# Optimization experiments

Hardware: AMD Instinct MI355X
Metric: run time of the kernel (lower is better)

Reference implementation:

```python
import jax, jax.numpy as jnp
import numpy as np

# Dims: N tokens, D input, H expert hidden, O output, E experts, G gate hidden, K top-k
N, D, H, O, E, G, K = 8192, 1024, 2048, 1024, 8, 256, 2
BALANCE_COEF = 0.01


def setup_inputs() -> dict:
    key = jax.random.key(0)
    ks = jax.random.split(key, 12)
    def lin(k, shape, fan_in):
        return jax.random.normal(k, shape, jnp.float32) * (1.0 / np.sqrt(fan_in))
    return {
        "x":   jax.random.normal(ks[0], (N, D), jnp.float32),
        # gating MLP: D -> G -> E
        "Wg1": lin(ks[1], (D, G), D), "bg1": jnp.zeros((G,), jnp.float32),
        "Wg2": lin(ks[2], (G, E), G), "bg2": jnp.zeros((E,), jnp.float32),
        # stacked expert MLPs: D -> H -> H -> O (ExpertNetwork, num_layers=2)
        "W1": lin(ks[3], (E, D, H), D), "b1": jnp.zeros((E, H), jnp.float32),
        "W2": lin(ks[4], (E, H, H), H), "b2": jnp.zeros((E, H), jnp.float32),
        "W3": lin(ks[5], (E, H, O), H), "b3": jnp.zeros((E, O), jnp.float32),
    }


def reference(x, Wg1, bg1, Wg2, bg2, W1, b1, W2, b2, W3, b3):
    # Gating: 2-layer MLP -> softmax -> top-k -> renormalize (eval: no noise/dropout)
    logits = jnp.maximum(x @ Wg1 + bg1, 0.0) @ Wg2 + bg2            # [N, E]
    probs = jax.nn.softmax(logits, axis=-1)
    w, idx = jax.lax.top_k(probs, K)                                # [N, K]
    w = w / jnp.sum(w, axis=-1, keepdims=True)
    onehot = jax.nn.one_hot(idx, E, dtype=x.dtype)                  # [N, K, E]
    comb = jnp.sum(onehot * w[..., None], axis=1)                   # [N, E] per-token expert weight

    # Dense-equivalent combine: unselected tokens get weight 0, identical math to
    # the masked dispatch + scatter-add in the torch code.
    def expert_step(acc, params):
        W1e, b1e, W2e, b2e, W3e, b3e, we = params                   # we: [N]
        h = jnp.maximum(x @ W1e + b1e, 0.0)                         # [N, H]
        h = jnp.maximum(h @ W2e + b2e, 0.0)                         # [N, H]
        o = h @ W3e + b3e                                           # [N, O]
        return acc + o * we[:, None], None

    out, _ = jax.lax.scan(expert_step, jnp.zeros((N, O), x.dtype),
                          (W1, b1, W2, b2, W3, b3, comb.T))

    # aux losses: expert_usage[e] = sum_i mean_b(indices[b,i]==e)
    expert_usage = jnp.sum(onehot, axis=(0, 1)) / N                 # [E]
    balance_loss = jnp.mean((expert_usage - 1.0 / E) ** 2) * BALANCE_COEF
    return out, balance_loss, expert_usage
```

## Files before the change

### kernel.cpp

```cpp
#include <hip/hip_runtime.h>
#include <hip/hip_bf16.h>
#include <cstdint>
#include <cstddef>

#define N_TOK 8192
#define D_IN  1024
#define H_DIM 2048
#define O_DIM 1024
#define E_NUM 8
#define G_DIM 256
#define MAXT256 72
#define MAXT128 144
#define MAXROWS (MAXT256*256)

typedef __attribute__((ext_vector_type(8))) __bf16 bf16x8;
typedef __attribute__((ext_vector_type(4))) float floatx4;

#define GCAST(p) ((__attribute__((address_space(1))) void*)(void*)(p))
#define LCAST(p) ((__attribute__((address_space(3))) void*)(p))

#define JOB_G1_END   512
#define JOB_CAST_END 4608
#define JOB_W1_END   8704

__device__ inline void transpose_body(const float* __restrict__ src,
                                      __bf16* __restrict__ dst,
                                      int K, int N, int e, int ktile, int ntile,
                                      float* smemf) {
  float (*tl)[64] = (float(*)[64])smemf;
  const float* s = src + (size_t)e * K * N;
  __bf16* d = dst + (size_t)e * K * N;
  int k0 = ktile * 64, n0 = ntile * 64;
  int t = threadIdx.x;
  int kr = t >> 4, nc = t & 15;
#pragma unroll
  for (int p = 0; p < 4; p++) {
    int r = kr + p * 16;
    float4 v = *reinterpret_cast<const float4*>(
        s + (size_t)(k0 + r) * N + n0 + nc * 4);
    *reinterpret_cast<float4*>(&tl[r][(nc * 4 + 8 * (r >> 3)) & 63]) = v;
  }
  __syncthreads();
  int n = t >> 3, kg = t & 7;
#pragma unroll
  for (int p = 0; p < 2; p++) {
    int c = n + p * 32;
    bf16x8 o;
#pragma unroll
    for (int j = 0; j < 8; j++)
      o[j] = (__bf16)tl[kg * 8 + j][(c + 8 * kg) & 63];
    *reinterpret_cast<bf16x8*>(d + (size_t)(n0 + c) * K + k0 + kg * 8) = o;
  }
}

__device__ inline void gate1_body(const float* __restrict__ x,
                                  const float* __restrict__ Wg1,
                                  const float* __restrict__ bg1,
                                  float* __restrict__ g,
                                  int bn, int bm, float* smemf) {
  float (*As)[68] = (float(*)[68])smemf;
  float (*Bs)[68] = (float(*)[68])(smemf + 32 * 68);
  int t = threadIdx.x;
  int tm = t >> 4, tn = t & 15;
  float acc[4][4] = {};
  for (int k0 = 0; k0 < D_IN; k0 += 32) {
#pragma unroll
    for (int i = 0; i < 2; i++) {
      int idx = t + 256 * i;
      int row = idx >> 3, c4 = idx & 7;
      float4 v = *reinterpret_cast<const float4*>(
          x + (size_t)(bm * 64 + row) * D_IN + k0 + c4 * 4);
      As[c4 * 4 + 0][row] = v.x;
      As[c4 * 4 + 1][row] = v.y;
      As[c4 * 4 + 2][row] = v.z;
      As[c4 * 4 + 3][row] = v.w;
      int brow = idx >> 4, bc4 = idx & 15;
      float4 wv = *reinterpret_cast<const float4*>(
          Wg1 + (size_t)(k0 + brow) * G_DIM + bn * 64 + bc4 * 4);
      *reinterpret_cast<float4*>(&Bs[brow][bc4 * 4]) = wv;
    }
    __syncthreads();
#pragma unroll
    for (int k = 0; k < 32; k++) {
      float4 av = *reinterpret_cast<const float4*>(&As[k][tm * 4]);
      float4 bv = *reinterpret_cast<const float4*>(&Bs[k][tn * 4]);
      float a4[4] = {av.x, av.y, av.z, av.w};
      float b4[4] = {bv.x, bv.y, bv.z, bv.w};
#pragma unroll
      for (int r = 0; r < 4; r++)
#pragma unroll
        for (int c = 0; c < 4; c++) acc[r][c] = fmaf(a4[r], b4[c], acc[r][c]);
    }
    __syncthreads();
  }
  int gr = bm * 64 + tm * 4, gc = bn * 64 + tn * 4;
#pragma unroll
  for (int r = 0; r < 4; r++) {
    float4 o;
    o.x = fmaxf(acc[r][0] + bg1[gc + 0], 0.f);
    o.y = fmaxf(acc[r][1] + bg1[gc + 1], 0.f);
    o.z = fmaxf(acc[r][2] + bg1[gc + 2], 0.f);
    o.w = fmaxf(acc[r][3] + bg1[gc + 3], 0.f);
    *reinterpret_cast<float4*>(g + (size_t)(gr + r) * G_DIM + gc) = o;
  }
}

__global__ __launch_bounds__(256) void prep_kernel(
    const float* __restrict__ x, __bf16* __restrict__ xb,
    const float* __restrict__ W1, __bf16* __restrict__ W1t,
    const float* __restrict__ Wg1, const float* __restrict__ bg1,
    float* __restrict__ g) {
  __shared__ float smemf[4352];
  int b = blockIdx.x;
  if (b < JOB_G1_END) {
    gate1_body(x, Wg1, bg1, g, b & 3, b >> 2, smemf);
  } else if (b < JOB_CAST_END) {
    int id = b - JOB_G1_END;
    int i = id * 2048 + threadIdx.x * 8;
    float4 v0 = *reinterpret_cast<const float4*>(x + i);
    float4 v1 = *reinterpret_cast<const float4*>(x + i + 4);
    bf16x8 o;
    o[0] = (__bf16)v0.x; o[1] = (__bf16)v0.y; o[2] = (__bf16)v0.z; o[3] = (__bf16)v0.w;
    o[4] = (__bf16)v1.x; o[5] = (__bf16)v1.y; o[6] = (__bf16)v1.z; o[7] = (__bf16)v1.w;
    *reinterpret_cast<bf16x8*>(xb + i) = o;
  } else {
    int id = b - JOB_CAST_END;
    transpose_body(W1, W1t, D_IN, H_DIM, id >> 9, (id >> 5) & 15, id & 31, smemf);
  }
}

__global__ __launch_bounds__(256) void gate2_kernel(const float* __restrict__ g,
                                                    const float* __restrict__ Wg2,
                                                    const float* __restrict__ bg2,
                                                    int* __restrict__ top_idx,
                                                    float* __restrict__ top_w,
                                                    int* __restrict__ counts) {
  __shared__ float lg[32][9];
  int t = threadIdx.x;
  int tl = t >> 3, e = t & 7;
  int n = blockIdx.x * 32 + tl;
  const float* gr = g + (size_t)n * G_DIM;
  float acc = bg2[e];
  for (int i = 0; i < G_DIM; i += 4) {
    float4 v = *reinterpret_cast<const float4*>(gr + i);
    acc += v.x * Wg2[(i + 0) * E_NUM + e];
    acc += v.y * Wg2[(i + 1) * E_NUM + e];
    acc += v.z * Wg2[(i + 2) * E_NUM + e];
    acc += v.w * Wg2[(i + 3) * E_NUM + e];
  }
  lg[tl][e] = acc;
  __syncthreads();
  if (e == 0) {
    float l[8];
#pragma unroll
    for (int i = 0; i < 8; i++) l[i] = lg[tl][i];
    int i0 = 0;
    for (int i = 1; i < 8; i++)
      if (l[i] > l[i0]) i0 = i;
    int i1 = (i0 == 0) ? 1 : 0;
    for (int i = 0; i < 8; i++)
      if (i != i0 && l[i] > l[i1]) i1 = i;
    float d = expf(l[i1] - l[i0]);
    float w0 = 1.f / (1.f + d);
    float w1 = d * w0;
    top_idx[n * 2 + 0] = i0;
    top_idx[n * 2 + 1] = i1;
    top_w[n * 2 + 0] = w0;
    top_w[n * 2 + 1] = w1;
    atomicAdd(&counts[i0], 1);
    atomicAdd(&counts[i1], 1);
  }
}

__global__ void g3_kernel(const int* __restrict__ counts, int* __restrict__ cursors,
                          int* __restrict__ off_pad, int* __restrict__ nt128,
                          int* __restrict__ nt256,
                          int* __restrict__ meta128, int* __restrict__ meta256,
                          float* __restrict__ out_tail,
                          int* __restrict__ slot_token) {
  if (threadIdx.x == 0) {
    int off = 0, n2 = 0, n1 = 0;
    float mse = 0.f;
    for (int e = 0; e < E_NUM; e++) {
      off_pad[e] = off;
      int c = counts[e];
      int tiles = (c + 255) >> 8;
      for (int i = 0; i < tiles; i++) {
        int s0 = off + i * 256;
        meta256[n2 * 2 + 0] = e; meta256[n2 * 2 + 1] = s0; n2++;
        meta128[n1 * 2 + 0] = e; meta128[n1 * 2 + 1] = s0; n1++;
        meta128[n1 * 2 + 0] = e; meta128[n1 * 2 + 1] = s0 + 128; n1++;
      }
      off += tiles << 8;
      cursors[e] = 0;
      float u = (float)c / (float)N_TOK;
      out_tail[1 + e] = u;
      float dd = u - 0.125f;
      mse += dd * dd;
    }
    *nt256 = n2;
    *nt128 = n1;
    out_tail[0] = (mse / 8.0f) * 0.01f;
  }
  for (int s = threadIdx.x; s < MAXROWS; s += 256) slot_token[s] = 0;
}

__global__ __launch_bounds__(256) void scatter_kernel(const int* __restrict__ top_idx,
                                                      const int* __restrict__ off_pad,
                                                      int* __restrict__ cursors,
                                                      int* __restrict__ slot_token,
                                                      int* __restrict__ token_slots) {
  int n = blockIdx.x * 256 + threadIdx.x;
#pragma unroll
  for (int k = 0; k < 2; k++) {
    int e = top_idx[n * 2 + k];
    int pos = atomicAdd(&cursors[e], 1);
    int s = off_pad[e] + pos;
    slot_token[s] = n;
    token_slots[n * 2 + k] = s;
  }
}

__global__ __launch_bounds__(256) void moe_gemm_kernel(
    const __bf16* __restrict__ A, int Astride,
    const __bf16* __restrict__ Wt, const float* __restrict__ bias,
    int Kdim, int Ndim,
    const int* __restrict__ tile_meta, const int* __restrict__ ntiles_p,
    const int* __restrict__ slot_token,
    __bf16* __restrict__ h_out,
    const float* __restrict__ W2src, __bf16* __restrict__ W2dst,
    const float* __restrict__ W3src, __bf16* __restrict__ W3dst) {
  __shared__ __align__(16) char smem[32768];
  int tile = blockIdx.y;
  if (tile >= MAXT128) {
    int id = (tile - MAXT128) * gridDim.x + blockIdx.x;
    if (id < 8192) {
      transpose_body(W2src, W2dst, H_DIM, H_DIM, id >> 10, (id >> 5) & 31,
                     id & 31, (float*)smem);
    } else {
      id -= 8192;
      transpose_body(W3src, W3dst, H_DIM, O_DIM, id >> 9, (id >> 4) & 31,
                     id & 15, (float*)smem);
    }
    return;
  }
  if (tile >= *ntiles_p) return;
  __bf16* As = (__bf16*)smem;
  __bf16* Bs = (__bf16*)(smem + 16384);
  int ex = tile_meta[tile * 2 + 0];
  int slot0 = tile_meta[tile * 2 + 1];
  int n0 = blockIdx.x * 128;
  int t = threadIdx.x, l = t & 63, w = t >> 6;

  size_t aoff[4], boff[4];
#pragma unroll
  for (int i = 0; i < 4; i++) {
    int gidx = (w * 4 + i) * 64 + l;
    int row = gidx >> 3;
    int kch = (gidx & 7) ^ (row & 7);
    int sl = slot0 + row;
    long long rb = (long long)slot_token[sl] * Astride;
    aoff[i] = (size_t)rb + kch * 8;
    boff[i] = ((size_t)ex * Ndim + n0 + row) * (size_t)Kdim + kch * 8;
  }

  int wm = (w >> 1) * 64, wn = (w & 1) * 64;
  int lm = l & 15, lq = l >> 4;
  floatx4 acc[4][4] = {};

  for (int k0 = 0; k0 < Kdim; k0 += 64) {
#pragma unroll
    for (int i = 0; i < 4; i++) {
      __builtin_amdgcn_global_load_lds(GCAST(A + aoff[i] + k0),
                                       LCAST((char*)As + w * 4096 + i * 1024),
                                       16, 0, 0);
      __builtin_amdgcn_global_load_lds(GCAST(Wt + boff[i] + k0),
                                       LCAST((char*)Bs + w * 4096 + i * 1024),
                                       16, 0, 0);
    }
    __syncthreads();
#pragma unroll
    for (int half = 0; half < 2; half++) {
      bf16x8 af[4], bfr[4];
#pragma unroll
      for (int i = 0; i < 4; i++) {
        int r = wm + i * 16 + lm;
        int s = (half * 4 + lq) ^ (r & 7);
        af[i] = *reinterpret_cast<const bf16x8*>(As + r * 64 + s * 8);
      }
#pragma unroll
      for (int j = 0; j < 4; j++) {
        int r = wn + j * 16 + lm;
        int s = (half * 4 + lq) ^ (r & 7);
        bfr[j] = *reinterpret_cast<const bf16x8*>(Bs + r * 64 + s * 8);
      }
#pragma unroll
      for (int i = 0; i < 4; i++)
#pragma unroll
        for (int j = 0; j < 4; j++)
          acc[i][j] = __builtin_amdgcn_mfma_f32_16x16x32_bf16(af[i], bfr[j],
                                                              acc[i][j], 0, 0, 0);
    }
    __syncthreads();
  }

  float bcol[4];
#pragma unroll
  for (int j = 0; j < 4; j++) bcol[j] = bias[(size_t)ex * Ndim + n0 + wn + j * 16 + lm];
#pragma unroll
  for (int i = 0; i < 4; i++) {
#pragma unroll
    for (int r = 0; r < 4; r++) {
      int sl = slot0 + wm + i * 16 + lq * 4 + r;
      __bf16* hrow = h_out + (size_t)sl * Ndim + n0 + wn + lm;
#pragma unroll
      for (int j = 0; j < 4; j++) {
        float v = fmaxf(acc[i][j][r] + bcol[j], 0.f);
        hrow[j * 16] = (__bf16)v;
      }
    }
  }
}

__global__ __launch_bounds__(512) void moe_gemm256_kernel(
    const __bf16* __restrict__ A,
    const __bf16* __restrict__ Wt, const float* __restrict__ bias,
    int Kdim, int Ndim,
    const int* __restrict__ tile_meta, const int* __restrict__ ntiles_p,
    __bf16* __restrict__ h_out, float* __restrict__ y_out, int finalMode) {
  __shared__ __align__(16) char smem[131072];
  int tile = blockIdx.y;
  if (tile >= *ntiles_p) return;
  int ex = tile_meta[tile * 2 + 0];
  int slot0 = tile_meta[tile * 2 + 1];
  int n0 = blockIdx.x * 256;
  int t = threadIdx.x, l = t & 63, w = t >> 6;
  int wm2 = w >> 2, wn4 = w & 3;
  int lm = l & 15, lq = l >> 4;

  size_t aoff[2][2], boff[2][2];
#pragma unroll
  for (int h = 0; h < 2; h++)
#pragma unroll
    for (int i = 0; i < 2; i++) {
      int gidx = i * 512 + t;
      int row = gidx >> 3;
      int kch = (gidx & 7) ^ (row & 7);
      aoff[h][i] = (size_t)(slot0 + h * 128 + row) * (size_t)Kdim + kch * 8;
      boff[h][i] = ((size_t)ex * Ndim + n0 + h * 128 + row) * (size_t)Kdim + kch * 8;
    }

  floatx4 acc[8][4] = {};

  auto SA = [&](int kt, int h, int d) {
    char* dst = smem + d * 65536 + h * 16384;
#pragma unroll
    for (int i = 0; i < 2; i++)
      __builtin_amdgcn_global_load_lds(GCAST(A + aoff[h][i] + (size_t)kt * 64),
                                       LCAST(dst + i * 8192 + w * 1024), 16, 0, 0);
  };
  auto SB = [&](int kt, int h, int d) {
    char* dst = smem + d * 65536 + 32768 + h * 16384;
#pragma unroll
    for (int i = 0; i < 2; i++)
      __builtin_amdgcn_global_load_lds(GCAST(Wt + boff[h][i] + (size_t)kt * 64),
                                       LCAST(dst + i * 8192 + w * 1024), 16, 0, 0);
  };

  int NKT = Kdim >> 6;
  int NIT = NKT >> 1;

  asm volatile("s_waitcnt vmcnt(0)" ::: "memory");
  SA(0, 0, 0); SA(0, 1, 0); SB(0, 0, 0); SB(0, 1, 0);
  SB(1, 0, 1); SB(1, 1, 1);
  asm volatile("s_waitcnt vmcnt(4)" ::: "memory");
  __builtin_amdgcn_s_barrier();
  __builtin_amdgcn_sched_barrier(0);

#pragma unroll 1
  for (int it = 0; it < NIT; ++it) {
    int kt1 = 2 * it + 1, kt2 = 2 * it + 2, kt3 = 2 * it + 3;
    bool last = (it == NIT - 1);
    bf16x8 bfr[4][2];

#pragma unroll
    for (int q = 0; q < 4; q++) {
      bf16x8 af[2][2];
      const __bf16* As = (const __bf16*)(smem);
      const __bf16* Bsl = (const __bf16*)(smem + 32768);
      if (q == 0) {
#pragma unroll
        for (int j = 0; j < 4; j++) {
          int c = wn4 * 64 + j * 16 + lm;
#pragma unroll
          for (int ks = 0; ks < 2; ks++)
            bfr[j][ks] = *reinterpret_cast<const bf16x8*>(Bsl + c * 64 + ((ks * 4 + lq) ^ (c & 7)) * 8);
        }
      }
#pragma unroll
      for (int ii = 0; ii < 2; ii++) {
        int r = wm2 * 128 + (q * 2 + ii) * 16 + lm;
#pragma unroll
        for (int ks = 0; ks < 2; ks++)
          af[ii][ks] = *reinterpret_cast<const bf16x8*>(As + r * 64 + ((ks * 4 + lq) ^ (r & 7)) * 8);
      }
      if (q == 0) SA(kt1, 0, 1);
      else if (q == 1) SA(kt1, 1, 1);
      else if (q == 2) { if (kt2 < NKT) SB(kt2, 0, 0); }
      else             { if (kt2 < NKT) SB(kt2, 1, 0); }
      __builtin_amdgcn_s_barrier();
      asm volatile("s_waitcnt lgkmcnt(0)" ::: "memory");
      __builtin_amdgcn_sched_barrier(0);
      __builtin_amdgcn_s_setprio(1);
#pragma unroll
      for (int ii = 0; ii < 2; ii++)
#pragma unroll
        for (int j = 0; j < 4; j++)
#pragma unroll
          for (int ks = 0; ks < 2; ks++)
            acc[q * 2 + ii][j] = __builtin_amdgcn_mfma_f32_16x16x32_bf16(
                af[ii][ks], bfr[j][ks], acc[q * 2 + ii][j], 0, 0, 0);
      __builtin_amdgcn_s_setprio(0);
      if (q == 3) {
        if (last) asm volatile("s_waitcnt vmcnt(0)" ::: "memory");
        else      asm volatile("s_waitcnt vmcnt(4)" ::: "memory");
      }
      __builtin_amdgcn_s_barrier();
      __builtin_amdgcn_sched_barrier(0);
    }

#pragma unroll
    for (int q = 0; q < 4; q++) {
      bf16x8 af[2][2];
      const __bf16* As = (const __bf16*)(smem + 65536);
      const __bf16* Bsl = (const __bf16*)(smem + 65536 + 32768);
      if (q == 0) {
#pragma unroll
        for (int j = 0; j < 4; j++) {
          int c = wn4 * 64 + j * 16 + lm;
#pragma unroll
          for (int ks = 0; ks < 2; ks++)
            bfr[j][ks] = *reinterpret_cast<const bf16x8*>(Bsl + c * 64 + ((ks * 4 + lq) ^ (c & 7)) * 8);
        }
      }
#pragma unroll
      for (int ii = 0; ii < 2; ii++) {
        int r = wm2 * 128 + (q * 2 + ii) * 16 + lm;
#pragma unroll
        for (int ks = 0; ks < 2; ks++)
          af[ii][ks] = *reinterpret_cast<const bf16x8*>(As + r * 64 + ((ks * 4 + lq) ^ (r & 7)) * 8);
      }
      if (q == 0)      { if (kt2 < NKT) SA(kt2, 0, 0); }
      else if (q == 1) { if (kt2 < NKT) SA(kt2, 1, 0); }
      else if (q == 2) { if (kt3 < NKT) SB(kt3, 0, 1); }
      else             { if (kt3 < NKT) SB(kt3, 1, 1); }
      __builtin_amdgcn_s_barrier();
      asm volatile("s_waitcnt lgkmcnt(0)" ::: "memory");
      __builtin_amdgcn_sched_barrier(0);
      __builtin_amdgcn_s_setprio(1);
#pragma unroll
      for (int ii = 0; ii < 2; ii++)
#pragma unroll
        for (int j = 0; j < 4; j++)
#pragma unroll
          for (int ks = 0; ks < 2; ks++)
            acc[q * 2 + ii][j] = __builtin_amdgcn_mfma_f32_16x16x32_bf16(
                af[ii][ks], bfr[j][ks], acc[q * 2 + ii][j], 0, 0, 0);
      __builtin_amdgcn_s_setprio(0);
      if (q == 3 && !last) {
        asm volatile("s_waitcnt vmcnt(4)" ::: "memory");
      }
      __builtin_amdgcn_s_barrier();
      __builtin_amdgcn_sched_barrier(0);
    }
  }

  float bcol[4];
#pragma unroll
  for (int j = 0; j < 4; j++)
    bcol[j] = bias[(size_t)ex * Ndim + n0 + wn4 * 64 + j * 16 + lm];

  if (finalMode) {
#pragma unroll
    for (int i = 0; i < 8; i++) {
#pragma unroll
      for (int r = 0; r < 4; r++) {
        int sl = slot0 + wm2 * 128 + i * 16 + lq * 4 + r;
        float* yrow = y_out + (size_t)sl * Ndim + n0 + wn4 * 64 + lm;
#pragma unroll
        for (int j = 0; j < 4; j++) yrow[j * 16] = acc[i][j][r] + bcol[j];
      }
    }
  } else {
#pragma unroll
    for (int i = 0; i < 8; i++) {
#pragma unroll
      for (int r = 0; r < 4; r++) {
        int sl = slot0 + wm2 * 128 + i * 16 + lq * 4 + r;
        __bf16* hrow = h_out + (size_t)sl * Ndim + n0 + wn4 * 64 + lm;
#pragma unroll
        for (int j = 0; j < 4; j++) {
          float v = fmaxf(acc[i][j][r] + bcol[j], 0.f);
          hrow[j * 16] = (__bf16)v;
        }
      }
    }
  }
}

__global__ __launch_bounds__(256) void combine_kernel(const float* __restrict__ y,
                                                      const int* __restrict__ token_slots,
                                                      const float* __restrict__ top_w,
                                                      float* __restrict__ out) {
  int n = blockIdx.x;
  int t = threadIdx.x;
  int s0 = token_slots[n * 2 + 0], s1 = token_slots[n * 2 + 1];
  float w0 = top_w[n * 2 + 0], w1 = top_w[n * 2 + 1];
  float4 a = reinterpret_cast<const float4*>(y + (size_t)s0 * O_DIM)[t];
  float4 b = reinterpret_cast<const float4*>(y + (size_t)s1 * O_DIM)[t];
  float4 o;
  o.x = w0 * a.x + w1 * b.x;
  o.y = w0 * a.y + w1 * b.y;
  o.z = w0 * a.z + w1 * b.z;
  o.w = w0 * a.w + w1 * b.w;
  reinterpret_cast<float4*>(out + (size_t)n * O_DIM)[t] = o;
}

extern "C" void kernel_launch(void* const* d_in, const int* in_sizes, int n_in,
                              void* d_out, int out_size, void* d_ws, size_t ws_size,
                              hipStream_t stream) {
  const float* x   = (const float*)d_in[0];
  const float* Wg1 = (const float*)d_in[1];
  const float* bg1 = (const float*)d_in[2];
  const float* Wg2 = (const float*)d_in[3];
  const float* bg2 = (const float*)d_in[4];
  const float* W1  = (const float*)d_in[5];
  const float* b1  = (const float*)d_in[6];
  const float* W2  = (const float*)d_in[7];
  const float* b2  = (const float*)d_in[8];
  const float* W3  = (const float*)d_in[9];
  const float* b3  = (const float*)d_in[10];
  float* out = (float*)d_out;

  char* ws = (char*)d_ws;
  __bf16* x_bf       = (__bf16*)(ws + 0);
  __bf16* W1t        = (__bf16*)(ws + 16777216);
  __bf16* W2t        = (__bf16*)(ws + 50331648);
  __bf16* W3t        = (__bf16*)(ws + 117440512);
  __bf16* h1         = (__bf16*)(ws + 150994944);
  __bf16* h2         = (__bf16*)(ws + 226492416);
  float*  y          = (float*) (ws + 16777216);
  float*  gbuf       = (float*) (ws + 226492416);
  int*    top_idx    = (int*)   (ws + 301989888);
  float*  top_w      = (float*) (ws + 302055424);
  int*    slot_token = (int*)   (ws + 302120960);
  int*    token_slots= (int*)   (ws + 302194688);
  int*    meta       = (int*)   (ws + 302260224);
  int* counts    = meta;
  int* cursors   = meta + 8;
  int* off_pad   = meta + 16;
  int* nt128     = meta + 24;
  int* nt256     = meta + 25;
  int* meta128   = meta + 32;
  int* meta256   = meta + 320;
  float* out_tail = out + (size_t)N_TOK * O_DIM;

  hipMemsetAsync(meta, 0, 64, stream);

  prep_kernel<<<JOB_W1_END, 256, 0, stream>>>(x, x_bf, W1, W1t, Wg1, bg1, gbuf);
  gate2_kernel<<<N_TOK / 32, 256, 0, stream>>>(gbuf, Wg2, bg2, top_idx, top_w, counts);
  g3_kernel<<<1, 256, 0, stream>>>(counts, cursors, off_pad, nt128, nt256,
                                   meta128, meta256, out_tail, slot_token);
  scatter_kernel<<<N_TOK / 256, 256, 0, stream>>>(top_idx, off_pad, cursors,
                                                  slot_token, token_slots);

  moe_gemm_kernel<<<dim3(H_DIM / 128, MAXT128 + 768), 256, 0, stream>>>(
      x_bf, D_IN, W1t, b1, D_IN, H_DIM, meta128, nt128, slot_token,
      h1, W2, W2t, W3, W3t);
  moe_gemm256_kernel<<<dim3(H_DIM / 256, MAXT256), 512, 0, stream>>>(
      h1, W2t, b2, H_DIM, H_DIM, meta256, nt256, h2, nullptr, 0);
  moe_gemm256_kernel<<<dim3(O_DIM / 256, MAXT256), 512, 0, stream>>>(
      h2, W3t, b3, H_DIM, O_DIM, meta256, nt256, nullptr, y, 1);
  combine_kernel<<<N_TOK, 256, 0, stream>>>(y, token_slots, top_w, out);
}
```

Baseline: 975.9 us.

## Retile W2 GEMM to 256x128 with triple-buffered A and move W3 to 128-tile kernel

The second expert GEMM now uses 256x128 output tiles with a three-stage ring of A buffers and double-buffered B, instead of 256x256 tiles with two full stages. This doubles the number of column blocks, giving more work groups to fill the CUs. The third GEMM moves to the simpler 128x128 kernel through a new non-gather A path and an fp32 output mode. In exchange, each tile has lower arithmetic intensity, A panels are reloaded more often, and the hand-written vmcnt accounting is new and could be wrong.

```diff
diff --git a/kernel.cpp b/kernel.cpp
--- a/kernel.cpp
+++ b/kernel.cpp
@@ -222,12 +222,12 @@
 }
 
 __global__ __launch_bounds__(256) void moe_gemm_kernel(
-    const __bf16* __restrict__ A, int Astride,
+    const __bf16* __restrict__ A, int Astride, int gatherA,
     const __bf16* __restrict__ Wt, const float* __restrict__ bias,
     int Kdim, int Ndim,
     const int* __restrict__ tile_meta, const int* __restrict__ ntiles_p,
     const int* __restrict__ slot_token,
-    __bf16* __restrict__ h_out,
+    __bf16* __restrict__ h_out, float* __restrict__ y_out, int finalMode,
     const float* __restrict__ W2src, __bf16* __restrict__ W2dst,
     const float* __restrict__ W3src, __bf16* __restrict__ W3dst) {
   __shared__ __align__(16) char smem[32768];
@@ -259,7 +259,8 @@
     int row = gidx >> 3;
     int kch = (gidx & 7) ^ (row & 7);
     int sl = slot0 + row;
-    long long rb = (long long)slot_token[sl] * Astride;
+    long long rb = gatherA ? (long long)slot_token[sl] * Astride
+                           : (long long)sl * Astride;
     aoff[i] = (size_t)rb + kch * 8;
     boff[i] = ((size_t)ex * Ndim + n0 + row) * (size_t)Kdim + kch * 8;
   }
@@ -307,38 +308,52 @@
   float bcol[4];
 #pragma unroll
   for (int j = 0; j < 4; j++) bcol[j] = bias[(size_t)ex * Ndim + n0 + wn + j * 16 + lm];
-#pragma unroll
-  for (int i = 0; i < 4; i++) {
-#pragma unroll
-    for (int r = 0; r < 4; r++) {
-      int sl = slot0 + wm + i * 16 + lq * 4 + r;
-      __bf16* hrow = h_out + (size_t)sl * Ndim + n0 + wn + lm;
-#pragma unroll
-      for (int j = 0; j < 4; j++) {
-        float v = fmaxf(acc[i][j][r] + bcol[j], 0.f);
-        hrow[j * 16] = (__bf16)v;
-      }
-    }
-  }
-}
-
-__global__ __launch_bounds__(512) void moe_gemm256_kernel(
+
+  if (finalMode) {
+#pragma unroll
+    for (int i = 0; i < 4; i++) {
+#pragma unroll
+      for (int r = 0; r < 4; r++) {
+        int sl = slot0 + wm + i * 16 + lq * 4 + r;
+        float* yrow = y_out + (size_t)sl * Ndim + n0 + wn + lm;
+#pragma unroll
+        for (int j = 0; j < 4; j++) yrow[j * 16] = acc[i][j][r] + bcol[j];
+      }
+    }
+  } else {
+#pragma unroll
+    for (int i = 0; i < 4; i++) {
+#pragma unroll
+      for (int r = 0; r < 4; r++) {
+        int sl = slot0 + wm + i * 16 + lq * 4 + r;
+        __bf16* hrow = h_out + (size_t)sl * Ndim + n0 + wn + lm;
+#pragma unroll
+        for (int j = 0; j < 4; j++) {
+          float v = fmaxf(acc[i][j][r] + bcol[j], 0.f);
+          hrow[j * 16] = (__bf16)v;
+        }
+      }
+    }
+  }
+}
+
+__global__ __launch_bounds__(512) void moe_gemm2_kernel(
     const __bf16* __restrict__ A,
     const __bf16* __restrict__ Wt, const float* __restrict__ bias,
     int Kdim, int Ndim,
     const int* __restrict__ tile_meta, const int* __restrict__ ntiles_p,
-    __bf16* __restrict__ h_out, float* __restrict__ y_out, int finalMode) {
+    __bf16* __restrict__ h_out) {
   __shared__ __align__(16) char smem[131072];
   int tile = blockIdx.y;
   if (tile >= *ntiles_p) return;
   int ex = tile_meta[tile * 2 + 0];
   int slot0 = tile_meta[tile * 2 + 1];
-  int n0 = blockIdx.x * 256;
+  int n0 = blockIdx.x * 128;
   int t = threadIdx.x, l = t & 63, w = t >> 6;
-  int wm2 = w >> 2, wn4 = w & 3;
+  int wm4 = w >> 1, wn2 = w & 1;
   int lm = l & 15, lq = l >> 4;
 
-  size_t aoff[2][2], boff[2][2];
+  size_t aoff[2][2], boff[2];
 #pragma unroll
   for (int h = 0; h < 2; h++)
 #pragma unroll
@@ -347,67 +362,108 @@
       int row = gidx >> 3;
       int kch = (gidx & 7) ^ (row & 7);
       aoff[h][i] = (size_t)(slot0 + h * 128 + row) * (size_t)Kdim + kch * 8;
-      boff[h][i] = ((size_t)ex * Ndim + n0 + h * 128 + row) * (size_t)Kdim + kch * 8;
-    }
-
-  floatx4 acc[8][4] = {};
-
-  auto SA = [&](int kt, int h, int d) {
-    char* dst = smem + d * 65536 + h * 16384;
+    }
+#pragma unroll
+  for (int i = 0; i < 2; i++) {
+    int gidx = i * 512 + t;
+    int row = gidx >> 3;
+    int kch = (gidx & 7) ^ (row & 7);
+    boff[i] = ((size_t)ex * Ndim + n0 + row) * (size_t)Kdim + kch * 8;
+  }
+
+  floatx4 acc[4][4] = {};
+
+  auto SA = [&](int kt, int h, int sel) {
+    char* dst = smem + sel * 32768 + h * 16384;
 #pragma unroll
     for (int i = 0; i < 2; i++)
       __builtin_amdgcn_global_load_lds(GCAST(A + aoff[h][i] + (size_t)kt * 64),
                                        LCAST(dst + i * 8192 + w * 1024), 16, 0, 0);
   };
-  auto SB = [&](int kt, int h, int d) {
-    char* dst = smem + d * 65536 + 32768 + h * 16384;
+  auto SB = [&](int kt) {
+    char* dst = smem + 98304 + (kt & 1) * 16384;
 #pragma unroll
     for (int i = 0; i < 2; i++)
-      __builtin_amdgcn_global_load_lds(GCAST(Wt + boff[h][i] + (size_t)kt * 64),
+      __builtin_amdgcn_global_load_lds(GCAST(Wt + boff[i] + (size_t)kt * 64),
                                        LCAST(dst + i * 8192 + w * 1024), 16, 0, 0);
   };
+  auto PHASE = [&](const __bf16* Ab, const __bf16* Bb, int qb,
+                   bf16x8 (&bfr)[4][2], bool loadB) {
+    bf16x8 af[2][2];
+    if (loadB) {
+#pragma unroll
+      for (int j = 0; j < 4; j++) {
+        int c = wn2 * 64 + j * 16 + lm;
+#pragma unroll
+        for (int ks = 0; ks < 2; ks++)
+          bfr[j][ks] = *reinterpret_cast<const bf16x8*>(
+              Bb + c * 64 + ((ks * 4 + lq) ^ (c & 7)) * 8);
+      }
+    }
+#pragma unroll
+    for (int ii = 0; ii < 2; ii++) {
+      int r = wm4 * 64 + (qb + ii) * 16 + lm;
+      int half = r >> 7, rl = r & 127;
+#pragma unroll
+      for (int ks = 0; ks < 2; ks++)
+        af[ii][ks] = *reinterpret_cast<const bf16x8*>(
+            Ab + half * 8192 + rl * 64 + ((ks * 4 + lq) ^ (rl & 7)) * 8);
+    }
+    return af[0][0], af;
+  };
+  (void)PHASE;
 
   int NKT = Kdim >> 6;
   int NIT = NKT >> 1;
 
   asm volatile("s_waitcnt vmcnt(0)" ::: "memory");
-  SA(0, 0, 0); SA(0, 1, 0); SB(0, 0, 0); SB(0, 1, 0);
-  SB(1, 0, 1); SB(1, 1, 1);
-  asm volatile("s_waitcnt vmcnt(4)" ::: "memory");
+  SA(0, 0, 0); SA(0, 1, 0); SB(0);
+  SA(1, 0, 1); SA(1, 1, 1); SB(1);
+  asm volatile("s_waitcnt vmcnt(6)" ::: "memory");
   __builtin_amdgcn_s_barrier();
   __builtin_amdgcn_sched_barrier(0);
 
+  int sA = 0;
 #pragma unroll 1
   for (int it = 0; it < NIT; ++it) {
-    int kt1 = 2 * it + 1, kt2 = 2 * it + 2, kt3 = 2 * it + 3;
+    int kt2 = 2 * it + 2, kt3 = 2 * it + 3;
     bool last = (it == NIT - 1);
+    int s0 = sA, s1 = (sA + 1 > 2) ? 0 : sA + 1, s2 = (sA + 2 > 2) ? sA - 1 : sA + 2;
+    const __bf16* A0 = (const __bf16*)(smem + s0 * 32768);
+    const __bf16* A1 = (const __bf16*)(smem + s1 * 32768);
+    const __bf16* B0 = (const __bf16*)(smem + 98304);
+    const __bf16* B1 = (const __bf16*)(smem + 98304 + 16384);
     bf16x8 bfr[4][2];
 
 #pragma unroll
-    for (int q = 0; q < 4; q++) {
+    for (int P = 0; P < 4; P++) {
+      const __bf16* Ab = (P < 2) ? A0 : A1;
+      const __bf16* Bb = (P < 2) ? B0 : B1;
+      int qb = (P & 1) * 2;
       bf16x8 af[2][2];
-      const __bf16* As = (const __bf16*)(smem);
-      const __bf16* Bsl = (const __bf16*)(smem + 32768);
-      if (q == 0) {
+      if ((P & 1) == 0) {
 #pragma unroll
         for (int j = 0; j < 4; j++) {
-          int c = wn4 * 64 + j * 16 + lm;
+          int c = wn2 * 64 + j * 16 + lm;
 #pragma unroll
           for (int ks = 0; ks < 2; ks++)
-            bfr[j][ks] = *reinterpret_cast<const bf16x8*>(Bsl + c * 64 + ((ks * 4 + lq) ^ (c & 7)) * 8);
+            bfr[j][ks] = *reinterpret_cast<const bf16x8*>(
+                Bb + c * 64 + ((ks * 4 + lq) ^ (c & 7)) * 8);
         }
       }
 #pragma unroll
       for (int ii = 0; ii < 2; ii++) {
-        int r = wm2 * 128 + (q * 2 + ii) * 16 + lm;
+        int r = wm4 * 64 + (qb + ii) * 16 + lm;
+        int half = r >> 7, rl = r & 127;
 #pragma unroll
         for (int ks = 0; ks < 2; ks++)
-          af[ii][ks] = *reinterpret_cast<const bf16x8*>(As + r * 64 + ((ks * 4 + lq) ^ (r & 7)) * 8);
-      }
-      if (q == 0) SA(kt1, 0, 1);
-      else if (q == 1) SA(kt1, 1, 1);
-      else if (q == 2) { if (kt2 < NKT) SB(kt2, 0, 0); }
-      else             { if (kt2 < NKT) SB(kt2, 1, 0); }
+          af[ii][ks] = *reinterpret_cast<const bf16x8*>(
+              Ab + half * 8192 + rl * 64 + ((ks * 4 + lq) ^ (rl & 7)) * 8);
+      }
+      if (P == 0)      { if (kt2 < NKT) SA(kt2, 0, s2); }
+      else if (P == 1) { if (kt2 < NKT) { SA(kt2, 1, s2); SB(kt2); } }
+      else if (P == 2) { if (kt3 < NKT) SA(kt3, 0, s0); }
+      else             { if (kt3 < NKT) { SA(kt3, 1, s0); SB(kt3); } }
       __builtin_amdgcn_s_barrier();
       asm volatile("s_waitcnt lgkmcnt(0)" ::: "memory");
       __builtin_amdgcn_sched_barrier(0);
@@ -418,91 +474,35 @@
         for (int j = 0; j < 4; j++)
 #pragma unroll
           for (int ks = 0; ks < 2; ks++)
-            acc[q * 2 + ii][j] = __builtin_amdgcn_mfma_f32_16x16x32_bf16(
-                af[ii][ks], bfr[j][ks], acc[q * 2 + ii][j], 0, 0, 0);
+            acc[qb + ii][j] = __builtin_amdgcn_mfma_f32_16x16x32_bf16(
+                af[ii][ks], bfr[j][ks], acc[qb + ii][j], 0, 0, 0);
       __builtin_amdgcn_s_setprio(0);
-      if (q == 3) {
+      if (P == 1) {
         if (last) asm volatile("s_waitcnt vmcnt(0)" ::: "memory");
-        else      asm volatile("s_waitcnt vmcnt(4)" ::: "memory");
+        else      asm volatile("s_waitcnt vmcnt(6)" ::: "memory");
+      } else if (P == 3 && !last) {
+        asm volatile("s_waitcnt vmcnt(6)" ::: "memory");
       }
       __builtin_amdgcn_s_barrier();
       __builtin_amdgcn_sched_barrier(0);
     }
-
-#pragma unroll
-    for (int q = 0; q < 4; q++) {
-      bf16x8 af[2][2];
-      const __bf16* As = (const __bf16*)(smem + 65536);
-      const __bf16* Bsl = (const __bf16*)(smem + 65536 + 32768);
-      if (q == 0) {
-#pragma unroll
-        for (int j = 0; j < 4; j++) {
-          int c = wn4 * 64 + j * 16 + lm;
-#pragma unroll
-          for (int ks = 0; ks < 2; ks++)
-            bfr[j][ks] = *reinterpret_cast<const bf16x8*>(Bsl + c * 64 + ((ks * 4 + lq) ^ (c & 7)) * 8);
-        }
-      }
-#pragma unroll
-      for (int ii = 0; ii < 2; ii++) {
-        int r = wm2 * 128 + (q * 2 + ii) * 16 + lm;
-#pragma unroll
-        for (int ks = 0; ks < 2; ks++)
-          af[ii][ks] = *reinterpret_cast<const bf16x8*>(As + r * 64 + ((ks * 4 + lq) ^ (r & 7)) * 8);
-      }
-      if (q == 0)      { if (kt2 < NKT) SA(kt2, 0, 0); }
-      else if (q == 1) { if (kt2 < NKT) SA(kt2, 1, 0); }
-      else if (q == 2) { if (kt3 < NKT) SB(kt3, 0, 1); }
-      else             { if (kt3 < NKT) SB(kt3, 1, 1); }
-      __builtin_amdgcn_s_barrier();
-      asm volatile("s_waitcnt lgkmcnt(0)" ::: "memory");
-      __builtin_amdgcn_sched_barrier(0);
-      __builtin_amdgcn_s_setprio(1);
-#pragma unroll
-      for (int ii = 0; ii < 2; ii++)
-#pragma unroll
-        for (int j = 0; j < 4; j++)
-#pragma unroll
-          for (int ks = 0; ks < 2; ks++)
-            acc[q * 2 + ii][j] = __builtin_amdgcn_mfma_f32_16x16x32_bf16(
-                af[ii][ks], bfr[j][ks], acc[q * 2 + ii][j], 0, 0, 0);
-      __builtin_amdgcn_s_setprio(0);
-      if (q == 3 && !last) {
-        asm volatile("s_waitcnt vmcnt(4)" ::: "memory");
-      }
-      __builtin_amdgcn_s_barrier();
-      __builtin_amdgcn_sched_barrier(0);
-    }
+    sA = s2;
   }
 
   float bcol[4];
 #pragma unroll
   for (int j = 0; j < 4; j++)
-    bcol[j] = bias[(size_t)ex * Ndim + n0 + wn4 * 64 + j * 16 + lm];
-
-  if (finalMode) {
-#pragma unroll
-    for (int i = 0; i < 8; i++) {
-#pragma unroll
-      for (int r = 0; r < 4; r++) {
-        int sl = slot0 + wm2 * 128 + i * 16 + lq * 4 + r;
-        float* yrow = y_out + (size_t)sl * Ndim + n0 + wn4 * 64 + lm;
-#pragma unroll
-        for (int j = 0; j < 4; j++) yrow[j * 16] = acc[i][j][r] + bcol[j];
-      }
-    }
-  } else {
-#pragma unroll
-    for (int i = 0; i < 8; i++) {
-#pragma unroll
-      for (int r = 0; r < 4; r++) {
-        int sl = slot0 + wm2 * 128 + i * 16 + lq * 4 + r;
-        __bf16* hrow = h_out + (size_t)sl * Ndim + n0 + wn4 * 64 + lm;
-#pragma unroll
-        for (int j = 0; j < 4; j++) {
-          float v = fmaxf(acc[i][j][r] + bcol[j], 0.f);
-          hrow[j * 16] = (__bf16)v;
-        }
+    bcol[j] = bias[(size_t)ex * Ndim + n0 + wn2 * 64 + j * 16 + lm];
+#pragma unroll
+  for (int i = 0; i < 4; i++) {
+#pragma unroll
+    for (int r = 0; r < 4; r++) {
+      int sl = slot0 + wm4 * 64 + i * 16 + lq * 4 + r;
+      __bf16* hrow = h_out + (size_t)sl * Ndim + n0 + wn2 * 64 + lm;
+#pragma unroll
+      for (int j = 0; j < 4; j++) {
+        float v = fmaxf(acc[i][j][r] + bcol[j], 0.f);
+        hrow[j * 16] = (__bf16)v;
       }
     }
   }
@@ -575,11 +575,12 @@
                                                   slot_token, token_slots);
 
   moe_gemm_kernel<<<dim3(H_DIM / 128, MAXT128 + 768), 256, 0, stream>>>(
-      x_bf, D_IN, W1t, b1, D_IN, H_DIM, meta128, nt128, slot_token,
-      h1, W2, W2t, W3, W3t);
-  moe_gemm256_kernel<<<dim3(H_DIM / 256, MAXT256), 512, 0, stream>>>(
-      h1, W2t, b2, H_DIM, H_DIM, meta256, nt256, h2, nullptr, 0);
-  moe_gemm256_kernel<<<dim3(O_DIM / 256, MAXT256), 512, 0, stream>>>(
-      h2, W3t, b3, H_DIM, O_DIM, meta256, nt256, nullptr, y, 1);
+      x_bf, D_IN, 1, W1t, b1, D_IN, H_DIM, meta128, nt128, slot_token,
+      h1, nullptr, 0, W2, W2t, W3, W3t);
+  moe_gemm2_kernel<<<dim3(H_DIM / 128, MAXT256), 512, 0, stream>>>(
+      h1, W2t, b2, H_DIM, H_DIM, meta256, nt256, h2);
+  moe_gemm_kernel<<<dim3(O_DIM / 128, MAXT128), 256, 0, stream>>>(
+      h2, H_DIM, 0, W3t, b3, H_DIM, O_DIM, meta128, nt128, slot_token,
+      nullptr, y, 1, nullptr, nullptr, nullptr, nullptr);
   combine_kernel<<<N_TOK, 256, 0, stream>>>(y, token_slots, top_w, out);
 }
```

Result: slower. 1.003 ms (+2.8%).
